# Kernel optimization log

Hardware: AMD Instinct MI355X
Metric: run time of the kernel (lower is better)

## Reference

```python
import jax, jax.numpy as jnp
import numpy as np

N = 20000          # nodes
DEG = 32           # avg degree / num_neighbors
E = N * DEG        # edges
D_IN = 64          # irreps_node_input dim
D_HID = 144        # irreps_node_hidden dim
D_OUT = 3          # irreps_node_out = 1x1o
D_SH = 9           # edge spherical harmonics, (lmax+1)^2
N_BASIS = 10       # number_of_basis
MUL = 64           # fc hidden width
ATTR = 4           # node_attr dim
NUM_NEIGHBORS = 32.0


def setup_inputs() -> dict:
    key = jax.random.key(0)
    ks = jax.random.split(key, 32)
    rn = lambda k, shape, scale: jax.random.normal(k, shape, jnp.float32) * scale
    inp = {}
    inp['x'] = rn(ks[0], (N, D_IN), 1.0)
    inp['node_attr'] = rn(ks[1], (N, ATTR), 1.0)
    inp['edge_attr'] = rn(ks[2], (E, D_SH), 1.0)
    inp['edge_length_embedding'] = jax.random.uniform(ks[3], (E, N_BASIS), jnp.float32)
    dims = [(D_IN, D_HID), (D_HID, D_HID), (D_HID, D_OUT)]
    i = 4
    for l, (di, do) in enumerate(dims):
        inp['A' + str(l)] = rn(ks[i], (di, do), di ** -0.5); i += 1
        inp['B' + str(l)] = rn(ks[i], (D_SH, do), D_SH ** -0.5); i += 1
        inp['W1_' + str(l)] = rn(ks[i], (N_BASIS, MUL), N_BASIS ** -0.5); i += 1
        inp['W2_' + str(l)] = rn(ks[i], (MUL, 2 * MUL), MUL ** -0.5); i += 1
        inp['W3_' + str(l)] = rn(ks[i], (2 * MUL, do), (2 * MUL) ** -0.5); i += 1
        inp['Wsc' + str(l)] = rn(ks[i], (di * ATTR, do), (di * ATTR) ** -0.5); i += 1
    inp['edge_src'] = jax.random.randint(ks[i], (E,), 0, N, jnp.int32); i += 1
    inp['edge_dst'] = jax.random.randint(ks[i], (E,), 0, N, jnp.int32)
    inp['batch'] = jnp.zeros((N,), jnp.int32)
    return inp


def _mp_layer(x, node_attr, sh, emb, src, dst, A, B, W1, W2, W3, Wsc):
    # One gather -> edge tensor-product (factorized, per-edge weights from
    # radial MLP) -> scatter layer, plus node_attr-modulated self-connection.
    n = x.shape[0]
    # radial weight network on edge length embedding: [E, d_out]
    gate = jax.nn.silu(jax.nn.silu(emb @ W1) @ W2) @ W3
    # factorized tensor product of gathered node feats with edge sph. harmonics
    msg = gate * (x[src] @ A) * (sh @ B)              # [E, d_out]
    agg = jax.ops.segment_sum(msg, dst, num_segments=n) / jnp.sqrt(NUM_NEIGHBORS)
    # self connection: tensor product of node features with node attributes
    sc = jnp.einsum('ni,nj->nij', x, node_attr).reshape(n, -1) @ Wsc  # [N, d_out]
    return sc + agg


def reference(x, node_attr, edge_attr, edge_length_embedding,
              A0, B0, W1_0, W2_0, W3_0, Wsc0,
              A1, B1, W1_1, W2_1, W3_1, Wsc1,
              A2, B2, W1_2, W2_2, W3_2, Wsc2,
              edge_src, edge_dst, batch):
    h = jax.nn.silu(_mp_layer(x, node_attr, edge_attr, edge_length_embedding,
                              edge_src, edge_dst, A0, B0, W1_0, W2_0, W3_0, Wsc0))
    h = jax.nn.silu(_mp_layer(h, node_attr, edge_attr, edge_length_embedding,
                              edge_src, edge_dst, A1, B1, W1_1, W2_1, W3_1, Wsc1))
    out = _mp_layer(h, node_attr, edge_attr, edge_length_embedding,
                    edge_src, edge_dst, A2, B2, W1_2, W2_2, W3_2, Wsc2)
    return out  # [N, 3]
```

## Files before the change

### kernel.cpp

```cpp
#include <hip/hip_runtime.h>
#include <hip/hip_bf16.h>

#define NN 20000
#define NE 640000
#define DSH 9
#define NB 10
#define ATTR 4

typedef __attribute__((ext_vector_type(8))) short bfrag8;
typedef __attribute__((ext_vector_type(4))) float f32x4;
typedef unsigned int u32;
typedef unsigned short u16;

constexpr float INV_SQRT_NB = 0.17677669529663687f;

__device__ __forceinline__ float silu_f(float x) {
    return x * __builtin_amdgcn_rcpf(1.0f + __expf(-x));
}

__device__ __forceinline__ u16 f2bf(float v) {
    union { __hip_bfloat16 h; u16 u; } c;
    c.h = __float2bfloat16(v);
    return c.u;
}

__device__ __forceinline__ f32x4 mfma16(bfrag8 a, bfrag8 b, f32x4 c) {
    return __builtin_amdgcn_mfma_f32_16x16x32_bf16(a, b, c, 0, 0, 0);
}

__global__ void count_k(const int* __restrict__ idx, int* __restrict__ cnt) {
    int i = blockIdx.x * blockDim.x + threadIdx.x;
    int st = gridDim.x * blockDim.x;
    for (; i < NE; i += st) atomicAdd(&cnt[idx[i]], 1);
}

__global__ void count2_k(const int* __restrict__ dst, const int* __restrict__ src,
                         int* __restrict__ cntD, int* __restrict__ cntS) {
    int i = blockIdx.x * blockDim.x + threadIdx.x;
    int st = gridDim.x * blockDim.x;
    for (; i < NE; i += st) {
        atomicAdd(&cntD[dst[i]], 1);
        atomicAdd(&cntS[src[i]], 1);
    }
}

__device__ __forceinline__ void scan_body(const int* __restrict__ cnt, int* __restrict__ ptr) {
    __shared__ int ssum[256];
    const int T = 256, t = threadIdx.x;
    const int strip = (NN + T - 1) / T;
    int base = t * strip, s = 0;
    for (int i = 0; i < strip; i++) { int idx = base + i; if (idx < NN) s += cnt[idx]; }
    ssum[t] = s; __syncthreads();
    for (int off = 1; off < T; off <<= 1) {
        int v = (t >= off) ? ssum[t - off] : 0;
        __syncthreads();
        ssum[t] += v;
        __syncthreads();
    }
    int run = (t == 0) ? 0 : ssum[t - 1];
    for (int i = 0; i < strip; i++) {
        int idx = base + i;
        if (idx < NN) { int c = cnt[idx]; ptr[idx] = run; run += c; }
    }
    if (t == T - 1) ptr[NN] = run;
}

__global__ void scan_k(const int* __restrict__ cnt, int* __restrict__ ptr) {
    scan_body(cnt, ptr);
}

__global__ void scan2_k(const int* __restrict__ cntD, int* __restrict__ ptrD,
                        const int* __restrict__ cntS, int* __restrict__ ptrS) {
    if (blockIdx.x == 0) scan_body(cntD, ptrD);
    else                 scan_body(cntS, ptrS);
}

__global__ void fill_k(const int* __restrict__ idx, const int* __restrict__ ptr,
                       int* __restrict__ cnt, int* __restrict__ pos) {
    int i = blockIdx.x * blockDim.x + threadIdx.x;
    int st = gridDim.x * blockDim.x;
    for (; i < NE; i += st) {
        int d = idx[i];
        int r = atomicAdd(&cnt[d], 1);
        pos[i] = ptr[d] + r;
    }
}

__global__ void fill2_k(const int* __restrict__ dst, const int* __restrict__ src,
                        const int* __restrict__ ptrD, const int* __restrict__ ptrS,
                        int* __restrict__ cntD, int* __restrict__ cntS,
                        int* __restrict__ pos, int* __restrict__ ordS) {
    int i = blockIdx.x * blockDim.x + threadIdx.x;
    int st = gridDim.x * blockDim.x;
    for (; i < NE; i += st) {
        int d = dst[i];
        pos[i] = ptrD[d] + atomicAdd(&cntD[d], 1);
        int s = src[i];
        ordS[ptrS[s] + atomicAdd(&cntS[s], 1)] = i;
    }
}

__global__ void permute_pack_g(const float* __restrict__ emb, const float* __restrict__ sh,
                               const int* __restrict__ src, const int* __restrict__ pos,
                               const int* __restrict__ ordS,
                               u16* __restrict__ embsh, int* __restrict__ srcS,
                               int* __restrict__ posD2)
{
    int s = blockIdx.x * blockDim.x + threadIdx.x;
    if (s >= NE) return;
    int e = ordS[s];
    u16* row = embsh + (size_t)s * 20;
    #pragma unroll
    for (int k = 0; k < NB; k++)  row[k]      = f2bf(emb[(size_t)e * NB + k]);
    #pragma unroll
    for (int k = 0; k < DSH; k++) row[NB + k] = f2bf(sh[(size_t)e * DSH + k]);
    row[19] = 0;
    srcS[s]  = src[e];
    posD2[s] = pos[e];
}

__global__ void pack_all(const float* __restrict__ W1_0, const float* __restrict__ W2_0,
                         const float* __restrict__ W3_0, const float* __restrict__ B0,
                         const float* __restrict__ W1_1, const float* __restrict__ W2_1,
                         const float* __restrict__ W3_1, const float* __restrict__ B1,
                         const float* __restrict__ W1_2, const float* __restrict__ W2_2,
                         const float* __restrict__ W3_2, const float* __restrict__ B2,
                         u16* __restrict__ w1f0, u16* __restrict__ w2f0,
                         u16* __restrict__ w3f0, u16* __restrict__ bf0,
                         u16* __restrict__ w1f1, u16* __restrict__ w2f1,
                         u16* __restrict__ w3f1, u16* __restrict__ bf1,
                         u16* __restrict__ w1f2, u16* __restrict__ w2f2,
                         u16* __restrict__ w3f2, u16* __restrict__ bf2)
{
    int tid = blockIdx.x * blockDim.x + threadIdx.x;
    int grp = tid >> 6, l = tid & 63;
    if (grp >= 155) return;
    const float* W; u16* out; int K, N, KS, local;
    if      (grp <   4) { W = W1_0; out = w1f0; K = 10;  N = 64;  KS = 1; local = grp;       }
    else if (grp <  20) { W = W2_0; out = w2f0; K = 64;  N = 128; KS = 2; local = grp - 4;   }
    else if (grp <  56) { W = W3_0; out = w3f0; K = 128; N = 144; KS = 4; local = grp - 20;  }
    else if (grp <  65) { W = B0;   out = bf0;  K = 9;   N = 144; KS = 1; local = grp - 56;  }
    else if (grp <  69) { W = W1_1; out = w1f1; K = 10;  N = 64;  KS = 1; local = grp - 65;  }
    else if (grp <  85) { W = W2_1; out = w2f1; K = 64;  N = 128; KS = 2; local = grp - 69;  }
    else if (grp < 121) { W = W3_1; out = w3f1; K = 128; N = 144; KS = 4; local = grp - 85;  }
    else if (grp < 130) { W = B1;   out = bf1;  K = 9;   N = 144; KS = 1; local = grp - 121; }
    else if (grp < 134) { W = W1_2; out = w1f2; K = 10;  N = 64;  KS = 1; local = grp - 130; }
    else if (grp < 150) { W = W2_2; out = w2f2; K = 64;  N = 128; KS = 2; local = grp - 134; }
    else if (grp < 154) { W = W3_2; out = w3f2; K = 128; N = 3;   KS = 4; local = grp - 150; }
    else                { W = B2;   out = bf2;  K = 9;   N = 3;   KS = 1; local = grp - 154; }
    int s = local % KS, t = local / KS;
    int kb = s * 32 + ((l >> 4) << 3);
    int n = t * 16 + (l & 15);
    #pragma unroll
    for (int j = 0; j < 8; j++) {
        int k = kb + j;
        float v = (k < K && n < N) ? W[(size_t)k * N + n] : 0.f;
        out[(size_t)(local * 64 + l) * 8 + j] = f2bf(v);
    }
}

template<int DI, int DO, int NT>
__global__ void node_prep(const float* __restrict__ xin,
                          const float* __restrict__ attr,
                          const float* __restrict__ A,
                          const float* __restrict__ Wsc,
                          float* __restrict__ xa,
                          float* __restrict__ agg)
{
    __shared__ float sx[NT][DI];
    __shared__ float sat[NT][ATTR];
    const int n0 = blockIdx.x * NT;
    for (int idx = threadIdx.x; idx < NT * DI; idx += blockDim.x)
        sx[idx / DI][idx % DI] = xin[(size_t)n0 * DI + idx];
    if (threadIdx.x < NT * ATTR)
        sat[threadIdx.x / ATTR][threadIdx.x % ATTR] = attr[(size_t)n0 * ATTR + threadIdx.x];
    __syncthreads();

    const int o = threadIdx.x;
    if (o < DO) {
        float at[NT][ATTR];
        #pragma unroll
        for (int n = 0; n < NT; n++) {
            at[n][0] = sat[n][0]; at[n][1] = sat[n][1];
            at[n][2] = sat[n][2]; at[n][3] = sat[n][3];
        }
        float accA[NT], accS[NT];
        #pragma unroll
        for (int n = 0; n < NT; n++) { accA[n] = 0.f; accS[n] = 0.f; }
        for (int i = 0; i < DI; i++) {
            float a  = A[(size_t)i * DO + o];
            float w0 = Wsc[(size_t)(i * 4 + 0) * DO + o];
            float w1 = Wsc[(size_t)(i * 4 + 1) * DO + o];
            float w2 = Wsc[(size_t)(i * 4 + 2) * DO + o];
            float w3 = Wsc[(size_t)(i * 4 + 3) * DO + o];
            #pragma unroll
            for (int n = 0; n < NT; n++) {
                float xi = sx[n][i];
                accA[n] = fmaf(xi, a, accA[n]);
                float s = fmaf(at[n][3], w3,
                          fmaf(at[n][2], w2,
                          fmaf(at[n][1], w1, at[n][0] * w0)));
                accS[n] = fmaf(xi, s, accS[n]);
            }
        }
        #pragma unroll
        for (int n = 0; n < NT; n++) {
            xa [(size_t)(n0 + n) * DO + o] = accA[n];
            agg[(size_t)(n0 + n) * DO + o] = accS[n];
        }
    }
}

#define T3STEP(T3)                                                             \
    {                                                                          \
        f32x4 shb = mfma16(a_sh, bff[(T3) * 64 + l], Z4);                      \
        f32x4 acc = mfma16(a_h2_0, w3f[((T3) * 4 + 0) * 64 + l], Z4);          \
        acc = mfma16(a_h2_1, w3f[((T3) * 4 + 1) * 64 + l], acc);               \
        acc = mfma16(a_h2_2, w3f[((T3) * 4 + 2) * 64 + l], acc);               \
        acc = mfma16(a_h2_3, w3f[((T3) * 4 + 3) * 64 + l], acc);               \
        const int n = (T3) * 16 + c;                                           \
        float v0 = acc[0] * shb[0] * xv[(T3) * 4 + 0] * INV_SQRT_NB;           \
        float v1 = acc[1] * shb[1] * xv[(T3) * 4 + 1] * INV_SQRT_NB;           \
        float v2 = acc[2] * shb[2] * xv[(T3) * 4 + 2] * INV_SQRT_NB;           \
        float v3 = acc[3] * shb[3] * xv[(T3) * 4 + 3] * INV_SQRT_NB;           \
        int m0 = g * 4;                                                        \
        int d0 = ((m0 + 0) * 96 + (n >> 1)) ^ (((m0 + 0) & 7) << 2);           \
        int d1 = ((m0 + 1) * 96 + (n >> 1)) ^ (((m0 + 1) & 7) << 2);           \
        int d2 = ((m0 + 2) * 96 + (n >> 1)) ^ (((m0 + 2) & 7) << 2);           \
        int d3 = ((m0 + 3) * 96 + (n >> 1)) ^ (((m0 + 3) & 7) << 2);           \
        ((u16*)(h2dw + d0))[n & 1] = f2bf(v0);                                 \
        ((u16*)(h2dw + d1))[n & 1] = f2bf(v1);                                 \
        ((u16*)(h2dw + d2))[n & 1] = f2bf(v2);                                 \
        ((u16*)(h2dw + d3))[n & 1] = f2bf(v3);                                 \
    }

template<int DO, int PK>
__global__ void __launch_bounds__(256)
edge_mfma(const float* __restrict__ emb, const float* __restrict__ sh,
          const u16* __restrict__ embsh,
          const int* __restrict__ src, const int* __restrict__ pos,
          const u16* __restrict__ W1f, const u16* __restrict__ W2f,
          const u16* __restrict__ W3f, const u16* __restrict__ Bf,
          const float* __restrict__ xa, u32* __restrict__ msgdw,
          float* __restrict__ msg3)
{
    __shared__ u32 ldsa[4 * 2400];
    const int wid = threadIdx.x >> 6;
    const int l   = threadIdx.x & 63;
    u32* Wl = ldsa + wid * 2400;
    float* embL  = (float*)Wl;
    float* shL   = (float*)(Wl + 160);
    int*   sidxL = (int*)(Wl + 304);
    int*   posL  = (int*)(Wl + 320);
    u32*   h1dw  = Wl + 352;
    u32*   h2dw  = Wl + 864;

    const bfrag8* w1f = (const bfrag8*)W1f;
    const bfrag8* w2f = (const bfrag8*)W2f;
    const bfrag8* w3f = (const bfrag8*)W3f;
    const bfrag8* bff = (const bfrag8*)Bf;

    const int g = l >> 4, c = l & 15;
    const int gwave = blockIdx.x * 4 + wid;
    const int nwave = gridDim.x * 4;
    const f32x4 Z4 = {0.f, 0.f, 0.f, 0.f};

    for (int it = gwave; it < NE / 16; it += nwave) {
        const int e0 = it * 16;
        if constexpr (PK) {
            const u32* ep = (const u32*)embsh + (size_t)e0 * 10;
            for (int idx = l; idx < 160; idx += 64) Wl[idx] = ep[idx];
            if (l < 16) { sidxL[l] = src[e0 + l]; posL[l] = pos[e0 + l]; }
        } else {
            const float* ep = emb + (size_t)e0 * NB;
            for (int idx = l; idx < 16 * NB; idx += 64) embL[idx] = ep[idx];
            const float* sp = sh + (size_t)e0 * DSH;
            for (int idx = l; idx < 16 * DSH; idx += 64) shL[idx] = sp[idx];
            if (l < 16) { sidxL[l] = src[e0 + l]; posL[l] = pos[e0 + l]; }
        }
        const int si0 = sidxL[g * 4 + 0], si1 = sidxL[g * 4 + 1];
        const int si2 = sidxL[g * 4 + 2], si3 = sidxL[g * 4 + 3];
        float xv[(DO == 144) ? 36 : 1];
        if constexpr (DO == 144) {
            const float* xr0 = xa + (size_t)si0 * 144;
            const float* xr1 = xa + (size_t)si1 * 144;
            const float* xr2 = xa + (size_t)si2 * 144;
            const float* xr3 = xa + (size_t)si3 * 144;
            #pragma unroll
            for (int t3 = 0; t3 < 9; t3++) {
                xv[t3 * 4 + 0] = xr0[t3 * 16 + c];
                xv[t3 * 4 + 1] = xr1[t3 * 16 + c];
                xv[t3 * 4 + 2] = xr2[t3 * 16 + c];
                xv[t3 * 4 + 3] = xr3[t3 * 16 + c];
            }
        }
        bfrag8 a_emb, a_sh;
        {
            const int kb = g << 3;
            if constexpr (PK) {
                const u16* rowp = (const u16*)Wl + c * 20;
                #pragma unroll
                for (int j = 0; j < 8; j++) {
                    int k = kb + j;
                    a_emb[j] = (short)((k < NB)  ? rowp[k]      : (u16)0);
                    a_sh[j]  = (short)((k < DSH) ? rowp[NB + k] : (u16)0);
                }
            } else {
                #pragma unroll
                for (int j = 0; j < 8; j++) {
                    int k = kb + j;
                    a_emb[j] = (short)((k < NB)  ? f2bf(embL[c * NB + k])  : (u16)0);
                    a_sh[j]  = (short)((k < DSH) ? f2bf(shL[c * DSH + k]) : (u16)0);
                }
            }
        }
        #pragma unroll
        for (int t = 0; t < 4; t++) {
            f32x4 acc = mfma16(a_emb, w1f[t * 64 + l], Z4);
            #pragma unroll
            for (int r = 0; r < 4; r++) {
                int m = g * 4 + r, n = t * 16 + c;
                int dw = (m * 32 + (n >> 1)) ^ ((m & 7) << 2);
                ((u16*)(h1dw + dw))[n & 1] = f2bf(silu_f(acc[r]));
            }
        }
        bfrag8 a_h1_0, a_h1_1;
        {
            int bb = c * 32 + g * 4, xr = (c & 7) << 2;
            a_h1_0 = *(const bfrag8*)(h1dw + ((bb +  0) ^ xr));
            a_h1_1 = *(const bfrag8*)(h1dw + ((bb + 16) ^ xr));
        }
        #pragma unroll
        for (int t2 = 0; t2 < 8; t2++) {
            f32x4 acc = mfma16(a_h1_0, w2f[(t2 * 2 + 0) * 64 + l], Z4);
            acc = mfma16(a_h1_1, w2f[(t2 * 2 + 1) * 64 + l], acc);
            #pragma unroll
            for (int r = 0; r < 4; r++) {
                int m = g * 4 + r, n = t2 * 16 + c;
                int dw = (m * 64 + (n >> 1)) ^ ((m & 7) << 2);
                ((u16*)(h2dw + dw))[n & 1] = f2bf(silu_f(acc[r]));
            }
        }
        bfrag8 a_h2_0, a_h2_1, a_h2_2, a_h2_3;
        {
            int bb = c * 64 + g * 4, xr = (c & 7) << 2;
            a_h2_0 = *(const bfrag8*)(h2dw + ((bb +  0) ^ xr));
            a_h2_1 = *(const bfrag8*)(h2dw + ((bb + 16) ^ xr));
            a_h2_2 = *(const bfrag8*)(h2dw + ((bb + 32) ^ xr));
            a_h2_3 = *(const bfrag8*)(h2dw + ((bb + 48) ^ xr));
        }

        if constexpr (DO == 144) {
            T3STEP(0) T3STEP(1) T3STEP(2)
            __builtin_amdgcn_sched_barrier(0);
            T3STEP(3) T3STEP(4) T3STEP(5)
            __builtin_amdgcn_sched_barrier(0);
            T3STEP(6) T3STEP(7) T3STEP(8)
            for (int i = l; i < 1152; i += 64) {
                int m = i / 72;
                int xq = i - m * 72;
                u32 v = h2dw[(m * 96 + xq) ^ ((m & 7) << 2)];
                msgdw[(size_t)posL[m] * 72 + xq] = v;
            }
        } else {
            const int p0 = posL[g * 4 + 0], p1 = posL[g * 4 + 1];
            const int p2 = posL[g * 4 + 2], p3 = posL[g * 4 + 3];
            f32x4 shb = mfma16(a_sh, bff[l], Z4);
            f32x4 acc = mfma16(a_h2_0, w3f[0 * 64 + l], Z4);
            acc = mfma16(a_h2_1, w3f[1 * 64 + l], acc);
            acc = mfma16(a_h2_2, w3f[2 * 64 + l], acc);
            acc = mfma16(a_h2_3, w3f[3 * 64 + l], acc);
            if (c < 3) {
                msg3[(size_t)p0 * 3 + c] = acc[0] * shb[0] * xa[(size_t)si0 * 3 + c] * INV_SQRT_NB;
                msg3[(size_t)p1 * 3 + c] = acc[1] * shb[1] * xa[(size_t)si1 * 3 + c] * INV_SQRT_NB;
                msg3[(size_t)p2 * 3 + c] = acc[2] * shb[2] * xa[(size_t)si2 * 3 + c] * INV_SQRT_NB;
                msg3[(size_t)p3 * 3 + c] = acc[3] * shb[3] * xa[(size_t)si3 * 3 + c] * INV_SQRT_NB;
            }
        }
    }
}

template<int ACT>
__global__ void gather144(const u32* __restrict__ msgdw,
                          const int* __restrict__ ptr,
                          const float* __restrict__ sc,
                          float* __restrict__ outb)
{
    const int lane = threadIdx.x & 63;
    const int gw = blockIdx.x * (blockDim.x >> 6) + (threadIdx.x >> 6);
    const int nw = gridDim.x * (blockDim.x >> 6);
    for (int n = gw; n < NN; n += nw) {
        const int s0 = ptr[n], s1 = ptr[n + 1];
        float a0 = 0.f, a1 = 0.f, b0 = 0.f, b1 = 0.f;
        for (int s = s0; s < s1; s++) {
            u32 u = msgdw[(size_t)s * 72 + lane];
            a0 += __uint_as_float(u << 16);
            a1 += __uint_as_float(u & 0xffff0000u);
            if (lane < 8) {
                u32 v = msgdw[(size_t)s * 72 + 64 + lane];
                b0 += __uint_as_float(v << 16);
                b1 += __uint_as_float(v & 0xffff0000u);
            }
        }
        size_t base = (size_t)n * 144;
        float2 sv = *(const float2*)&sc[base + 2 * lane];
        float v0 = sv.x + a0, v1 = sv.y + a1;
        if (ACT) { v0 = silu_f(v0); v1 = silu_f(v1); }
        *(float2*)&outb[base + 2 * lane] = make_float2(v0, v1);
        if (lane < 8) {
            float2 sw = *(const float2*)&sc[base + 128 + 2 * lane];
            float w0 = sw.x + b0, w1 = sw.y + b1;
            if (ACT) { w0 = silu_f(w0); w1 = silu_f(w1); }
            *(float2*)&outb[base + 128 + 2 * lane] = make_float2(w0, w1);
        }
    }
}

__global__ void gather3(const float* __restrict__ msg3,
                        const int* __restrict__ ptr,
                        float* __restrict__ outb)
{
    int t = blockIdx.x * blockDim.x + threadIdx.x;
    if (t >= NN * 3) return;
    int n = t / 3, o = t - 3 * n;
    float a = 0.f;
    for (int s = ptr[n]; s < ptr[n + 1]; s++) a += msg3[(size_t)s * 3 + o];
    outb[t] += a;
}

extern "C" void kernel_launch(void* const* d_in, const int* in_sizes, int n_in,
                              void* d_out, int out_size, void* d_ws, size_t ws_size,
                              hipStream_t stream) {
    const float* x    = (const float*)d_in[0];
    const float* attr = (const float*)d_in[1];
    const float* sh   = (const float*)d_in[2];
    const float* emb  = (const float*)d_in[3];
    const float* A0   = (const float*)d_in[4];
    const float* B0   = (const float*)d_in[5];
    const float* W1_0 = (const float*)d_in[6];
    const float* W2_0 = (const float*)d_in[7];
    const float* W3_0 = (const float*)d_in[8];
    const float* Wsc0 = (const float*)d_in[9];
    const float* A1   = (const float*)d_in[10];
    const float* B1   = (const float*)d_in[11];
    const float* W1_1 = (const float*)d_in[12];
    const float* W2_1 = (const float*)d_in[13];
    const float* W3_1 = (const float*)d_in[14];
    const float* Wsc1 = (const float*)d_in[15];
    const float* A2   = (const float*)d_in[16];
    const float* B2   = (const float*)d_in[17];
    const float* W1_2 = (const float*)d_in[18];
    const float* W2_2 = (const float*)d_in[19];
    const float* W3_2 = (const float*)d_in[20];
    const float* Wsc2 = (const float*)d_in[21];
    const int*   src  = (const int*)d_in[22];
    const int*   dst  = (const int*)d_in[23];
    float* out = (float*)d_out;

    char* wp = (char*)d_ws;
    auto alloc = [&](size_t bytes) -> void* {
        void* r = (void*)wp;
        wp += (bytes + 255) & ~(size_t)255;
        return r;
    };
    float* xa   = (float*)alloc((size_t)NN * 144 * 4);
    float* agg  = (float*)alloc((size_t)NN * 144 * 4);
    float* hb   = (float*)alloc((size_t)NN * 144 * 4);
    int*   cnt2 = (int*)alloc((size_t)2 * NN * 4);
    int*   cnt  = cnt2;
    int*   cntS = cnt2 + NN;
    int*   ptr  = (int*)alloc((size_t)(NN + 1) * 4);
    int*   pos  = (int*)alloc((size_t)NE * 4);
    u16* w1f0 = (u16*)alloc(4 * 64 * 8 * 2);
    u16* w2f0 = (u16*)alloc(16 * 64 * 8 * 2);
    u16* w3f0 = (u16*)alloc(36 * 64 * 8 * 2);
    u16* bf0  = (u16*)alloc(9 * 64 * 8 * 2);
    u16* w1f1 = (u16*)alloc(4 * 64 * 8 * 2);
    u16* w2f1 = (u16*)alloc(16 * 64 * 8 * 2);
    u16* w3f1 = (u16*)alloc(36 * 64 * 8 * 2);
    u16* bf1  = (u16*)alloc(9 * 64 * 8 * 2);
    u16* w1f2 = (u16*)alloc(4 * 64 * 8 * 2);
    u16* w2f2 = (u16*)alloc(16 * 64 * 8 * 2);
    u16* w3f2 = (u16*)alloc(4 * 64 * 8 * 2);
    u16* bf2  = (u16*)alloc(1 * 64 * 8 * 2);
    char* msgbase = (char*)alloc((size_t)NE * 288);
    u32*   msgdw = (u32*)msgbase;
    float* msg3  = (float*)msgbase;
    u16* embshS = (u16*)alloc((size_t)NE * 20 * 2);
    int* srcS   = (int*)alloc((size_t)NE * 4);
    int* posD2  = (int*)alloc((size_t)NE * 4);
    size_t sort_need = (size_t)(wp - (char*)d_ws);
    const bool sorted = (ws_size >= sort_need);
    int* ordS = (int*)msgbase;
    int* ptrS = (int*)(msgbase + (size_t)NE * 4 + 256);

    if (sorted) {
        hipMemsetAsync(cnt2, 0, (size_t)2 * NN * 4, stream);
        count2_k<<<1024, 256, 0, stream>>>(dst, src, cnt, cntS);
        scan2_k<<<2, 256, 0, stream>>>(cnt, ptr, cntS, ptrS);
        hipMemsetAsync(cnt2, 0, (size_t)2 * NN * 4, stream);
        fill2_k<<<1024, 256, 0, stream>>>(dst, src, ptr, ptrS, cnt, cntS, pos, ordS);
        permute_pack_g<<<(NE + 255) / 256, 256, 0, stream>>>(
            emb, sh, src, pos, ordS, embshS, srcS, posD2);
    } else {
        hipMemsetAsync(cnt, 0, (size_t)NN * 4, stream);
        count_k<<<1024, 256, 0, stream>>>(dst, cnt);
        scan_k<<<1, 256, 0, stream>>>(cnt, ptr);
        hipMemsetAsync(cnt, 0, (size_t)NN * 4, stream);
        fill_k<<<1024, 256, 0, stream>>>(dst, ptr, cnt, pos);
    }

    pack_all<<<39, 256, 0, stream>>>(W1_0, W2_0, W3_0, B0, W1_1, W2_1, W3_1, B1,
                                     W1_2, W2_2, W3_2, B2,
                                     w1f0, w2f0, w3f0, bf0, w1f1, w2f1, w3f1, bf1,
                                     w1f2, w2f2, w3f2, bf2);

    if (sorted) {
        node_prep<64, 144, 8><<<NN / 8, 192, 0, stream>>>(x, attr, A0, Wsc0, xa, agg);
        edge_mfma<144, 1><<<2500, 256, 0, stream>>>(nullptr, nullptr, embshS, srcS, posD2,
            w1f0, w2f0, w3f0, bf0, xa, msgdw, nullptr);
        gather144<1><<<5000, 256, 0, stream>>>(msgdw, ptr, agg, hb);

        node_prep<144, 144, 8><<<NN / 8, 192, 0, stream>>>(hb, attr, A1, Wsc1, xa, agg);
        edge_mfma<144, 1><<<2500, 256, 0, stream>>>(nullptr, nullptr, embshS, srcS, posD2,
            w1f1, w2f1, w3f1, bf1, xa, msgdw, nullptr);
        gather144<1><<<5000, 256, 0, stream>>>(msgdw, ptr, agg, hb);

        node_prep<144, 3, 8><<<NN / 8, 192, 0, stream>>>(hb, attr, A2, Wsc2, xa, out);
        edge_mfma<3, 1><<<2500, 256, 0, stream>>>(nullptr, nullptr, embshS, srcS, posD2,
            w1f2, w2f2, w3f2, bf2, xa, nullptr, msg3);
        gather3<<<(NN * 3 + 255) / 256, 256, 0, stream>>>(msg3, ptr, out);
    } else {
        node_prep<64, 144, 8><<<NN / 8, 192, 0, stream>>>(x, attr, A0, Wsc0, xa, agg);
        edge_mfma<144, 0><<<2500, 256, 0, stream>>>(emb, sh, nullptr, src, pos,
            w1f0, w2f0, w3f0, bf0, xa, msgdw, nullptr);
        gather144<1><<<5000, 256, 0, stream>>>(msgdw, ptr, agg, hb);

        node_prep<144, 144, 8><<<NN / 8, 192, 0, stream>>>(hb, attr, A1, Wsc1, xa, agg);
        edge_mfma<144, 0><<<2500, 256, 0, stream>>>(emb, sh, nullptr, src, pos,
            w1f1, w2f1, w3f1, bf1, xa, msgdw, nullptr);
        gather144<1><<<5000, 256, 0, stream>>>(msgdw, ptr, agg, hb);

        node_prep<144, 3, 8><<<NN / 8, 192, 0, stream>>>(hb, attr, A2, Wsc2, xa, out);
        edge_mfma<3, 0><<<2500, 256, 0, stream>>>(emb, sh, nullptr, src, pos,
            w1f2, w2f2, w3f2, bf2, xa, nullptr, msg3);
        gather3<<<(NN * 3 + 255) / 256, 256, 0, stream>>>(msg3, ptr, out);
    }
}
```

Baseline: 1.112 ms.

## Fuse neighbor aggregation with next layer's node preparation kernel

Replaces the separate gather144 and node_prep launches between message-passing layers with one kernel, gnp. Each block segment-sums incoming messages for 8 nodes, adds the self-connection term and applies SiLU into shared memory. It then computes the next layer's A projection and attr-modulated self-connection from that shared tile. This removes a full round trip of the hidden node features through global memory and two kernel launches per layer boundary. In exchange, only 4 waves per block handle the irregular gather, and only the first DOUT threads do the dense part.

Measured after the change: 1.111 ms (median of 2 runs). Within noise of the previous version (-0.1%).

```diff
diff --git a/kernel.cpp b/kernel.cpp
--- a/kernel.cpp
+++ b/kernel.cpp
@@ -211,6 +211,83 @@
     }
 }
 
+template<int DOUT>
+__global__ void __launch_bounds__(256)
+gnp(const u32* __restrict__ msgdw, const int* __restrict__ ptr,
+    const float* __restrict__ sc, const float* __restrict__ attr,
+    const float* __restrict__ A, const float* __restrict__ Wsc,
+    float* __restrict__ xa, float* __restrict__ aggo)
+{
+    __shared__ float sx[8][144];
+    __shared__ float sat[8][ATTR];
+    const int n0 = blockIdx.x * 8;
+    const int wid = threadIdx.x >> 6, lane = threadIdx.x & 63;
+
+    #pragma unroll
+    for (int k = 0; k < 2; k++) {
+        const int nl = wid * 2 + k;
+        const int n = n0 + nl;
+        const int s0 = ptr[n], s1 = ptr[n + 1];
+        float a0 = 0.f, a1 = 0.f, b0 = 0.f, b1 = 0.f;
+        for (int s = s0; s < s1; s++) {
+            u32 u = msgdw[(size_t)s * 72 + lane];
+            a0 += __uint_as_float(u << 16);
+            a1 += __uint_as_float(u & 0xffff0000u);
+            if (lane < 8) {
+                u32 v = msgdw[(size_t)s * 72 + 64 + lane];
+                b0 += __uint_as_float(v << 16);
+                b1 += __uint_as_float(v & 0xffff0000u);
+            }
+        }
+        size_t base = (size_t)n * 144;
+        float2 sv = *(const float2*)&sc[base + 2 * lane];
+        sx[nl][2 * lane]     = silu_f(sv.x + a0);
+        sx[nl][2 * lane + 1] = silu_f(sv.y + a1);
+        if (lane < 8) {
+            float2 sw = *(const float2*)&sc[base + 128 + 2 * lane];
+            sx[nl][128 + 2 * lane] = silu_f(sw.x + b0);
+            sx[nl][129 + 2 * lane] = silu_f(sw.y + b1);
+        }
+    }
+    if (threadIdx.x < 8 * ATTR)
+        sat[threadIdx.x >> 2][threadIdx.x & 3] = attr[(size_t)n0 * ATTR + threadIdx.x];
+    __syncthreads();
+
+    const int o = threadIdx.x;
+    if (o < DOUT) {
+        float at[8][ATTR];
+        #pragma unroll
+        for (int n = 0; n < 8; n++) {
+            at[n][0] = sat[n][0]; at[n][1] = sat[n][1];
+            at[n][2] = sat[n][2]; at[n][3] = sat[n][3];
+        }
+        float accA[8], accS[8];
+        #pragma unroll
+        for (int n = 0; n < 8; n++) { accA[n] = 0.f; accS[n] = 0.f; }
+        for (int i = 0; i < 144; i++) {
+            float a  = A[(size_t)i * DOUT + o];
+            float w0 = Wsc[(size_t)(i * 4 + 0) * DOUT + o];
+            float w1 = Wsc[(size_t)(i * 4 + 1) * DOUT + o];
+            float w2 = Wsc[(size_t)(i * 4 + 2) * DOUT + o];
+            float w3 = Wsc[(size_t)(i * 4 + 3) * DOUT + o];
+            #pragma unroll
+            for (int n = 0; n < 8; n++) {
+                float xi = sx[n][i];
+                accA[n] = fmaf(xi, a, accA[n]);
+                float s = fmaf(at[n][3], w3,
+                          fmaf(at[n][2], w2,
+                          fmaf(at[n][1], w1, at[n][0] * w0)));
+                accS[n] = fmaf(xi, s, accS[n]);
+            }
+        }
+        #pragma unroll
+        for (int n = 0; n < 8; n++) {
+            xa  [(size_t)(n0 + n) * DOUT + o] = accA[n];
+            aggo[(size_t)(n0 + n) * DOUT + o] = accS[n];
+        }
+    }
+}
+
 #define T3STEP(T3)                                                             \
     {                                                                          \
         f32x4 shb = mfma16(a_sh, bff[(T3) * 64 + l], Z4);                      \
@@ -376,42 +453,6 @@
                 msg3[(size_t)p2 * 3 + c] = acc[2] * shb[2] * xa[(size_t)si2 * 3 + c] * INV_SQRT_NB;
                 msg3[(size_t)p3 * 3 + c] = acc[3] * shb[3] * xa[(size_t)si3 * 3 + c] * INV_SQRT_NB;
             }
-        }
-    }
-}
-
-template<int ACT>
-__global__ void gather144(const u32* __restrict__ msgdw,
-                          const int* __restrict__ ptr,
-                          const float* __restrict__ sc,
-                          float* __restrict__ outb)
-{
-    const int lane = threadIdx.x & 63;
-    const int gw = blockIdx.x * (blockDim.x >> 6) + (threadIdx.x >> 6);
-    const int nw = gridDim.x * (blockDim.x >> 6);
-    for (int n = gw; n < NN; n += nw) {
-        const int s0 = ptr[n], s1 = ptr[n + 1];
-        float a0 = 0.f, a1 = 0.f, b0 = 0.f, b1 = 0.f;
-        for (int s = s0; s < s1; s++) {
-            u32 u = msgdw[(size_t)s * 72 + lane];
-            a0 += __uint_as_float(u << 16);
-            a1 += __uint_as_float(u & 0xffff0000u);
-            if (lane < 8) {
-                u32 v = msgdw[(size_t)s * 72 + 64 + lane];
-                b0 += __uint_as_float(v << 16);
-                b1 += __uint_as_float(v & 0xffff0000u);
-            }
-        }
-        size_t base = (size_t)n * 144;
-        float2 sv = *(const float2*)&sc[base + 2 * lane];
-        float v0 = sv.x + a0, v1 = sv.y + a1;
-        if (ACT) { v0 = silu_f(v0); v1 = silu_f(v1); }
-        *(float2*)&outb[base + 2 * lane] = make_float2(v0, v1);
-        if (lane < 8) {
-            float2 sw = *(const float2*)&sc[base + 128 + 2 * lane];
-            float w0 = sw.x + b0, w1 = sw.y + b1;
-            if (ACT) { w0 = silu_f(w0); w1 = silu_f(w1); }
-            *(float2*)&outb[base + 128 + 2 * lane] = make_float2(w0, w1);
         }
     }
 }
@@ -515,35 +556,32 @@
                                      w1f0, w2f0, w3f0, bf0, w1f1, w2f1, w3f1, bf1,
                                      w1f2, w2f2, w3f2, bf2);
 
-    if (sorted) {
-        node_prep<64, 144, 8><<<NN / 8, 192, 0, stream>>>(x, attr, A0, Wsc0, xa, agg);
-        edge_mfma<144, 1><<<2500, 256, 0, stream>>>(nullptr, nullptr, embshS, srcS, posD2,
+    const u16* es = embshS;
+    const int* sS = srcS;
+    const int* pS = posD2;
+
+    node_prep<64, 144, 8><<<NN / 8, 192, 0, stream>>>(x, attr, A0, Wsc0, xa, agg);
+    if (sorted)
+        edge_mfma<144, 1><<<2500, 256, 0, stream>>>(nullptr, nullptr, es, sS, pS,
             w1f0, w2f0, w3f0, bf0, xa, msgdw, nullptr);
-        gather144<1><<<5000, 256, 0, stream>>>(msgdw, ptr, agg, hb);
-
-        node_prep<144, 144, 8><<<NN / 8, 192, 0, stream>>>(hb, attr, A1, Wsc1, xa, agg);
-        edge_mfma<144, 1><<<2500, 256, 0, stream>>>(nullptr, nullptr, embshS, srcS, posD2,
-            w1f1, w2f1, w3f1, bf1, xa, msgdw, nullptr);
-        gather144<1><<<5000, 256, 0, stream>>>(msgdw, ptr, agg, hb);
-
-        node_prep<144, 3, 8><<<NN / 8, 192, 0, stream>>>(hb, attr, A2, Wsc2, xa, out);
-        edge_mfma<3, 1><<<2500, 256, 0, stream>>>(nullptr, nullptr, embshS, srcS, posD2,
-            w1f2, w2f2, w3f2, bf2, xa, nullptr, msg3);
-        gather3<<<(NN * 3 + 255) / 256, 256, 0, stream>>>(msg3, ptr, out);
-    } else {
-        node_prep<64, 144, 8><<<NN / 8, 192, 0, stream>>>(x, attr, A0, Wsc0, xa, agg);
+    else
         edge_mfma<144, 0><<<2500, 256, 0, stream>>>(emb, sh, nullptr, src, pos,
             w1f0, w2f0, w3f0, bf0, xa, msgdw, nullptr);
-        gather144<1><<<5000, 256, 0, stream>>>(msgdw, ptr, agg, hb);
-
-        node_prep<144, 144, 8><<<NN / 8, 192, 0, stream>>>(hb, attr, A1, Wsc1, xa, agg);
+    gnp<144><<<NN / 8, 256, 0, stream>>>(msgdw, ptr, agg, attr, A1, Wsc1, xa, hb);
+
+    if (sorted)
+        edge_mfma<144, 1><<<2500, 256, 0, stream>>>(nullptr, nullptr, es, sS, pS,
+            w1f1, w2f1, w3f1, bf1, xa, msgdw, nullptr);
+    else
         edge_mfma<144, 0><<<2500, 256, 0, stream>>>(emb, sh, nullptr, src, pos,
             w1f1, w2f1, w3f1, bf1, xa, msgdw, nullptr);
-        gather144<1><<<5000, 256, 0, stream>>>(msgdw, ptr, agg, hb);
-
-        node_prep<144, 3, 8><<<NN / 8, 192, 0, stream>>>(hb, attr, A2, Wsc2, xa, out);
+    gnp<3><<<NN / 8, 256, 0, stream>>>(msgdw, ptr, hb, attr, A2, Wsc2, xa, out);
+
+    if (sorted)
+        edge_mfma<3, 1><<<2500, 256, 0, stream>>>(nullptr, nullptr, es, sS, pS,
+            w1f2, w2f2, w3f2, bf2, xa, nullptr, msg3);
+    else
         edge_mfma<3, 0><<<2500, 256, 0, stream>>>(emb, sh, nullptr, src, pos,
             w1f2, w2f2, w3f2, bf2, xa, nullptr, msg3);
-        gather3<<<(NN * 3 + 255) / 256, 256, 0, stream>>>(msg3, ptr, out);
-    }
-}
+    gather3<<<(NN * 3 + 255) / 256, 256, 0, stream>>>(msg3, ptr, out);
+}
```
